# Kernel optimization log

Hardware: AMD Instinct MI355X
Metric: run time of the kernel (lower is better)

## Reference

```python
import jax, jax.numpy as jnp
import numpy as np

B, T, D, H, L = 64, 512, 1024, 1024, 2


def _make_params(key, in_size, hidden):
    # 4 input-to-hidden and 4 hidden-to-hidden matrices, gate order (i, f, n, o),
    # concatenated along the output axis -> one GEMM per source per step.
    k1, k2 = jax.random.split(key)
    sx = (6.0 / (in_size + hidden)) ** 0.5   # xavier_uniform bound
    sh = (6.0 / (hidden + hidden)) ** 0.5
    Wx = jax.random.uniform(k1, (in_size, 4 * hidden), minval=-sx, maxval=sx, dtype=jnp.float32)
    Wh = jax.random.uniform(k2, (hidden, 4 * hidden), minval=-sh, maxval=sh, dtype=jnp.float32)
    b = jnp.zeros((4 * hidden,), dtype=jnp.float32)
    return Wx, Wh, b


def setup_inputs() -> dict:
    key = jax.random.key(0)
    kx, k0, k1 = jax.random.split(key, 3)
    x = jax.random.normal(kx, (B, T, D), dtype=jnp.float32)
    h0 = jnp.zeros((L, B, H), dtype=jnp.float32)
    c0 = jnp.zeros((L, B, H), dtype=jnp.float32)
    Wx0, Wh0, b0 = _make_params(k0, D, H)
    Wx1, Wh1, b1 = _make_params(k1, H, H)
    return {"x": x, "h0": h0, "c0": c0,
            "Wx0": Wx0, "Wh0": Wh0, "b0": b0,
            "Wx1": Wx1, "Wh1": Wh1, "b1": b1}


def _run_layer(xseq, h, c, Wx, Wh, b):
    # xseq: [T, B, in], h/c: [B, H]
    def step(carry, xt):
        h, c = carry
        g = xt @ Wx + h @ Wh + b                       # [B, 4H]
        i_t, f_t, n_t, o_t = jnp.split(g, 4, axis=-1)
        i_t = jax.nn.sigmoid(i_t)
        f_t = jax.nn.sigmoid(f_t)
        n_t = jnp.tanh(n_t)
        o_t = jax.nn.sigmoid(o_t)
        c = f_t * c + i_t * n_t
        h = o_t * jnp.tanh(c)
        return (h, c), h
    (h, c), ys = jax.lax.scan(step, (h, c), xseq)
    return ys, h, c                                     # ys: [T, B, H]


def reference(x, h0, c0, Wx0, Wh0, b0, Wx1, Wh1, b1):
    xs = jnp.transpose(x, (1, 0, 2))                    # [T, B, D]
    params = [(Wx0, Wh0, b0), (Wx1, Wh1, b1)]
    hs, cs = [], []
    for layer in range(L):
        Wx, Wh, b = params[layer]
        xs, h, c = _run_layer(xs, h0[layer], c0[layer], Wx, Wh, b)
        hs.append(h)
        cs.append(c)
    outputs = jnp.transpose(xs, (1, 0, 2))              # [B, T, H]
    return outputs, (jnp.stack(hs, 0), jnp.stack(cs, 0))
```

## Files before the change

kernel.cpp:

```cpp
#include <hip/hip_runtime.h>


#define NBLK 256
#define TPB  512
#define T_   512
#define HS_OFF 33554432
#define CS_OFF 33685504

typedef float  f32x4  __attribute__((ext_vector_type(4)));
typedef short  bf16x8 __attribute__((ext_vector_type(8)));

#define WS_CTR  0u
#define WS_W    139264u
#define WS_BIAS 33693696u
#define WS_XB   33726464u
#define WS_H0   100835328u
#define WS_H1   101097472u
#define WS_MIN  101359616u

__device__ __forceinline__ unsigned short f2bf(float f) {
  union { float f; unsigned u; } v; v.f = f;
  return (unsigned short)((v.u + 0x7FFFu + ((v.u >> 16) & 1u)) >> 16);
}
__device__ __forceinline__ float fsig(float x) { return 1.0f / (1.0f + __expf(-x)); }
__device__ __forceinline__ float ftanh(float x) {
  x = fminf(15.0f, fmaxf(-15.0f, x));
  float e = __expf(2.0f * x);
  return (e - 1.0f) / (e + 1.0f);
}

__global__ void kw(const float* __restrict__ Wx0, const float* __restrict__ Wh0,
                   const float* __restrict__ Wx1, const float* __restrict__ Wh1,
                   unsigned short* __restrict__ wp) {
  __shared__ float tile[64][65];
  int tb = blockIdx.x;
  int m  = tb >> 10;
  int kt = (tb >> 6) & 15;
  int nt = tb & 63;
  const float* W = (m == 0) ? Wx0 : (m == 1) ? Wh0 : (m == 2) ? Wx1 : Wh1;
  unsigned short* O = wp + (size_t)m * 4194304u;
  int k0 = kt * 64, n0 = nt * 64;
  int tx = threadIdx.x & 63, tg = threadIdx.x >> 6;
  for (int r = tg; r < 64; r += 4)
    tile[r][tx] = W[(size_t)(k0 + r) * 4096 + n0 + tx];
  __syncthreads();
  for (int r = tg; r < 64; r += 4) {
    int n = n0 + r;
    int p = ((n & 1023) << 2) | (n >> 10);
    O[(size_t)p * 1024 + k0 + tx] = f2bf(tile[tx][r]);
  }
}

__global__ void kx(const float* __restrict__ x, unsigned short* __restrict__ xb) {
  int row = blockIdx.x;
  int t = row >> 6, b = row & 63;
  const float4* src = (const float4*)(x + ((size_t)b * 512 + t) * 1024);
  float4 f = src[threadIdx.x];
  ushort4 o; o.x = f2bf(f.x); o.y = f2bf(f.y); o.z = f2bf(f.z); o.w = f2bf(f.w);
  ((ushort4*)(xb + (size_t)row * 1024))[threadIdx.x] = o;
}

__global__ void kmisc(const float* __restrict__ b0, const float* __restrict__ b1,
                      const float* __restrict__ h0in,
                      float* __restrict__ biasP,
                      unsigned short* __restrict__ h0r, unsigned short* __restrict__ h1r) {
  int idx = blockIdx.x * 256 + threadIdx.x;
  if (idx < 8192) {
    int layer = idx >> 12, p = idx & 4095;
    int orig = (p & 3) * 1024 + (p >> 2);
    biasP[idx] = (layer ? b1 : b0)[orig];
  } else if (idx < 139264) {
    int e = idx - 8192;
    int layer = e >> 16, o = e & 65535;
    int row = o >> 10, col = o & 1023;
    unsigned short v = f2bf(h0in[layer * 65536 + o]);
    int dst = 65536 + (col >> 3) * 512 + row * 8 + (col & 7);
    if (layer) h1r[dst] = v; else h0r[dst] = v;
  }
}

__global__ void __launch_bounds__(TPB, 2)
klstm(const float* __restrict__ c0_in,
      const unsigned short* __restrict__ wp,
      const float* __restrict__ biasP,
      const unsigned short* __restrict__ xb,
      unsigned short* __restrict__ h0ring,
      unsigned short* __restrict__ h1ring,
      unsigned* __restrict__ ctrbase,
      float* __restrict__ out) {
  extern __shared__ char smem[];
  float* red  = (float*)(smem + 131072);
  float* lhb  = (float*)(smem + 139264);
  float* xred = (float*)(smem + 141312);
  unsigned* gctr  = ctrbase;
  unsigned* rctr  = ctrbase + 16384;
  unsigned* gflag = ctrbase + 17408;
  const int tid = threadIdx.x;
  const int w   = tid >> 6;
  const int l   = tid & 63;
  const int bid = blockIdx.x;
  const int n0  = bid * 16;
  const int layer = w >> 2;
  const int rbase = (w & 3) * 16;
  const int khalf = (w >> 2) * 512;
  const int grp   = bid >> 4;
  float* lh = lhb + w * 64;

  {
    const int msrc[4] = {0, 2, 1, 3};
    for (int s = 0; s < 4; ++s) {
      const char* src = (const char*)(wp + (size_t)msrc[s] * 4194304u + (size_t)n0 * 1024u);
      char* dst = smem + s * 32768;
      for (int i = tid; i < 2048; i += TPB) {
        int sb = i << 4;
        int c  = sb >> 11;
        int kb = sb & 2047;
        *(uint4*)(dst + (c << 11) + (kb ^ ((c & 7) << 4))) = *(const uint4*)(src + sb);
      }
    }
  }

  const int jg = bid * 4 + ((l & 15) >> 2);
  const float biasv = biasP[layer * 4096 + n0 + (l & 15)];
  const int qb = l & ~3;

  float cr[4];
  #pragma unroll
  for (int v = 0; v < 4; ++v)
    cr[v] = c0_in[layer * 65536 + (rbase + (l >> 4) * 4 + v) * 1024 + jg];

  const int ae0  = (rbase + (l & 15)) * 1024 + khalf + (l >> 4) * 8;
  const int hbase = ((khalf >> 3) + (l >> 4)) * 512 + (rbase + (l & 15)) * 8;
  const int lb0  = (l & 15) << 11;
  const int kb2  = khalf * 2 + (l >> 4) * 16;
  const int swz  = (l & 7) << 4;
  const int hsto = (bid >> 1) * 512 + 4 * (bid & 1);

  __syncthreads();

  f32x4 xacc = {0.f, 0.f, 0.f, 0.f};
  {
    #pragma unroll
    for (int kk = 0; kk < 16; ++kk) {
      bf16x8 ax = *(const bf16x8*)(xb + ae0 + kk * 32);
      bf16x8 b  = *(const bf16x8*)(smem + lb0 + ((kb2 + kk * 64) ^ swz));
      xacc = __builtin_amdgcn_mfma_f32_16x16x32_bf16(ax, b, xacc, 0, 0, 0);
    }
    if (w >= 4) {
      float* xr = xred + (size_t)(w & 3) * 256 + (size_t)l * 4;
      #pragma unroll
      for (int v = 0; v < 4; ++v) xr[v] = xacc[v];
    }
  }
  __syncthreads();

  for (int k = 0; k <= T_; ++k) {
    const unsigned short* h0p = h0ring + ((k + 1) & 1) * 65536;
    const unsigned short* h1p = h1ring + (k & 1) * 65536;

    bf16x8 hf0[16], hf1[16];
    #pragma unroll
    for (int kk = 0; kk < 16; ++kk) {
      const unsigned short* a0p = h0p + hbase + kk * 2048;
      const unsigned short* a1p = h1p + hbase + kk * 2048;
      asm volatile("global_load_dwordx4 %0, %1, off sc0 sc1"
                   : "=v"(hf0[kk]) : "v"(a0p));
      asm volatile("global_load_dwordx4 %0, %1, off sc0 sc1"
                   : "=v"(hf1[kk]) : "v"(a1p));
    }
    asm volatile("s_waitcnt vmcnt(0)" ::: "memory");
    __builtin_amdgcn_sched_barrier(0);

    f32x4 acc0  = {0.f, 0.f, 0.f, 0.f};
    f32x4 acc1a = {0.f, 0.f, 0.f, 0.f};
    f32x4 acc1b = {0.f, 0.f, 0.f, 0.f};
    #pragma unroll
    for (int kk = 0; kk < 16; ++kk) {
      const int bo = lb0 + ((kb2 + kk * 64) ^ swz);
      bf16x8 bh0 = *(const bf16x8*)(smem + 65536 + bo);
      bf16x8 bx1 = *(const bf16x8*)(smem + 32768 + bo);
      bf16x8 bh1 = *(const bf16x8*)(smem + 98304 + bo);
      acc0  = __builtin_amdgcn_mfma_f32_16x16x32_bf16(hf0[kk], bh0, acc0, 0, 0, 0);
      acc1a = __builtin_amdgcn_mfma_f32_16x16x32_bf16(hf0[kk], bx1, acc1a, 0, 0, 0);
      acc1b = __builtin_amdgcn_mfma_f32_16x16x32_bf16(hf1[kk], bh1, acc1b, 0, 0, 0);
    }

    {
      float* rb = red + (size_t)(w * 64 + l) * 4;
      f32x4 other = layer ? acc0 : (acc1a + acc1b);
      #pragma unroll
      for (int v = 0; v < 4; ++v) rb[v] = other[v];
    }
    __syncthreads();

    f32x4 g = layer ? (acc1a + acc1b) : acc0;
    {
      const int pw = layer ? (w - 4) : (w + 4);
      const float* rb = red + (size_t)(pw * 64 + l) * 4;
      #pragma unroll
      for (int v = 0; v < 4; ++v) g[v] += rb[v];
    }
    if (w < 4) {
      const float* xr = xred + (size_t)w * 256 + (size_t)l * 4;
      #pragma unroll
      for (int v = 0; v < 4; ++v) g[v] += xacc[v] + xr[v];
    }

    const bool active = layer ? (k >= 1) : (k < T_);
    f32x4 outv = {0.f, 0.f, 0.f, 0.f};
    if (active) {
      unsigned short* hw = layer ? (h1ring + ((k + 1) & 1) * 65536)
                                 : (h0ring + (k & 1) * 65536);
      #pragma unroll
      for (int v = 0; v < 4; ++v) {
        float gv = g[v] + biasv;
        float gi = __shfl(gv, qb);
        float gf = __shfl(gv, qb | 1);
        float gn = __shfl(gv, qb | 2);
        float go = __shfl(gv, qb | 3);
        float i_ = fsig(gi), f_ = fsig(gf), n_ = ftanh(gn), o_ = fsig(go);
        float c = f_ * cr[v] + i_ * n_;
        cr[v] = c;
        float h = o_ * ftanh(c);
        if ((l & 3) == 0)
          lh[((l >> 4) * 4 + v) * 4 + ((l & 15) >> 2)] = h;
      }
      if (l < 16) {
        f32x4 h4 = *(f32x4*)(lh + l * 4);
        outv = h4;
        ushort4 u4;
        u4.x = f2bf(h4[0]); u4.y = f2bf(h4[1]); u4.z = f2bf(h4[2]); u4.w = f2bf(h4[3]);
        union { ushort4 s; unsigned long long q; } pk; pk.s = u4;
        __hip_atomic_store((unsigned long long*)(hw + hsto + (rbase + l) * 8), pk.q,
                           __ATOMIC_RELAXED, __HIP_MEMORY_SCOPE_AGENT);
      }
    }

    if (k < T_) {
      __syncthreads();
      if (tid == 0) {
        unsigned old = __hip_atomic_fetch_add(&gctr[grp * 1024 + k], 1u,
                                              __ATOMIC_RELAXED, __HIP_MEMORY_SCOPE_AGENT);
        if (old == 15u) {
          unsigned oldr = __hip_atomic_fetch_add(&rctr[k], 1u,
                                                 __ATOMIC_RELAXED, __HIP_MEMORY_SCOPE_AGENT);
          if (oldr == 15u) {
            #pragma unroll
            for (int gg = 0; gg < 16; ++gg)
              __hip_atomic_store(&gflag[gg * 1024 + k], 1u,
                                 __ATOMIC_RELAXED, __HIP_MEMORY_SCOPE_AGENT);
          }
        }
      }
    }

    if (active && l < 16) {
      const int row = rbase + l;
      if (layer) {
        *(f32x4*)(out + (size_t)row * 524288u + (size_t)(k - 1) * 1024u + bid * 4) = outv;
        if (k == T_)
          *(f32x4*)(out + HS_OFF + 65536 + row * 1024 + bid * 4) = outv;
      } else if (k == T_ - 1) {
        *(f32x4*)(out + HS_OFF + row * 1024 + bid * 4) = outv;
      }
    }
    if (k + 1 < T_) {
      const unsigned short* xt = xb + (size_t)(k + 1) * 65536u;
      f32x4 xa = {0.f, 0.f, 0.f, 0.f};
      #pragma unroll
      for (int kk = 0; kk < 16; ++kk) {
        bf16x8 ax = *(const bf16x8*)(xt + ae0 + kk * 32);
        bf16x8 b  = *(const bf16x8*)(smem + lb0 + ((kb2 + kk * 64) ^ swz));
        xa = __builtin_amdgcn_mfma_f32_16x16x32_bf16(ax, b, xa, 0, 0, 0);
      }
      if (w >= 4) {
        float* xr = xred + (size_t)(w & 3) * 256 + (size_t)l * 4;
        #pragma unroll
        for (int v = 0; v < 4; ++v) xr[v] = xa[v];
      } else {
        xacc = xa;
      }
    }

    if (k < T_) {
      if (tid == 0) {
        unsigned spins = 0;
        while (__hip_atomic_load(&gflag[grp * 1024 + k], __ATOMIC_RELAXED, __HIP_MEMORY_SCOPE_AGENT) == 0u) {
          __builtin_amdgcn_s_sleep(1);
          if (++spins > 67108864u) break;
        }
      }
      __syncthreads();
    }
  }

  if ((l & 3) == 0) {
    #pragma unroll
    for (int v = 0; v < 4; ++v)
      out[CS_OFF + layer * 65536 + (rbase + (l >> 4) * 4 + v) * 1024 + jg] = cr[v];
  }
}

extern "C" void kernel_launch(void* const* d_in, const int* in_sizes, int n_in,
                              void* d_out, int out_size, void* d_ws, size_t ws_size,
                              hipStream_t stream) {
  const float* x   = (const float*)d_in[0];
  const float* h0  = (const float*)d_in[1];
  const float* c0  = (const float*)d_in[2];
  const float* Wx0 = (const float*)d_in[3];
  const float* Wh0 = (const float*)d_in[4];
  const float* b0  = (const float*)d_in[5];
  const float* Wx1 = (const float*)d_in[6];
  const float* Wh1 = (const float*)d_in[7];
  const float* b1  = (const float*)d_in[8];
  float* out = (float*)d_out;
  char* ws = (char*)d_ws;
  if (ws_size < (size_t)WS_MIN) return;

  unsigned* ctr       = (unsigned*)(ws + WS_CTR);
  unsigned short* wp  = (unsigned short*)(ws + WS_W);
  float* biasP        = (float*)(ws + WS_BIAS);
  unsigned short* xbp = (unsigned short*)(ws + WS_XB);
  unsigned short* h0r = (unsigned short*)(ws + WS_H0);
  unsigned short* h1r = (unsigned short*)(ws + WS_H1);

  (void)hipMemsetAsync(ctr, 0, 139264, stream);
  hipLaunchKernelGGL(kw,    dim3(4096),  dim3(256), 0, stream, Wx0, Wh0, Wx1, Wh1, wp);
  hipLaunchKernelGGL(kx,    dim3(32768), dim3(256), 0, stream, x, xbp);
  hipLaunchKernelGGL(kmisc, dim3(544),   dim3(256), 0, stream, b0, b1, h0, biasP, h0r, h1r);

  (void)hipFuncSetAttribute((const void*)klstm, hipFuncAttributeMaxDynamicSharedMemorySize, 145408);
  const float* c0a = c0; const unsigned short* wpa = wp; const float* bpa = biasP;
  const unsigned short* xba = xbp;
  unsigned short* h0a = h0r; unsigned short* h1a = h1r;
  unsigned* ca = ctr; float* oa = out;
  void* args[] = {&c0a, &wpa, &bpa, &xba, &h0a, &h1a, &ca, &oa};
  hipError_t e = hipLaunchCooperativeKernel((const void*)klstm, dim3(NBLK), dim3(TPB),
                                            args, 145408, stream);
  if (e != hipSuccess) {
    hipLaunchKernelGGL(klstm, dim3(NBLK), dim3(TPB), 145408, stream,
                       c0a, wpa, bpa, xba, h0a, h1a, ca, oa);
  }
}
```

Before: 4.792 ms.

## Halve persistent LSTM grid, give each block 32 gate columns, stream Wx from global

```diff
diff --git a/kernel.cpp b/kernel.cpp
--- a/kernel.cpp
+++ b/kernel.cpp
@@ -1,7 +1,7 @@
 #include <hip/hip_runtime.h>
 
 
-#define NBLK 256
+#define NBLK 128
 #define TPB  512
 #define T_   512
 #define HS_OFF 33554432
@@ -11,12 +11,13 @@
 typedef short  bf16x8 __attribute__((ext_vector_type(8)));
 
 #define WS_CTR  0u
-#define WS_W    139264u
-#define WS_BIAS 33693696u
-#define WS_XB   33726464u
-#define WS_H0   100835328u
-#define WS_H1   101097472u
-#define WS_MIN  101359616u
+#define WS_W    69632u
+#define WS_WXF  33624064u
+#define WS_BIAS 50401280u
+#define WS_XB   50434048u
+#define WS_H0   117542912u
+#define WS_H1   117805056u
+#define WS_MIN  118067200u
 
 __device__ __forceinline__ unsigned short f2bf(float f) {
   union { float f; unsigned u; } v; v.f = f;
@@ -51,6 +52,20 @@
   }
 }
 
+__global__ void kwf(const unsigned short* __restrict__ wp, unsigned short* __restrict__ wxf) {
+  int unit = blockIdx.x * 4 + (threadIdx.x >> 6);
+  int lane = threadIdx.x & 63;
+  int m  = unit >> 13;
+  int r  = unit & 8191;
+  int g  = r >> 5;
+  int kh = (r >> 4) & 1;
+  int kk = r & 15;
+  const char* src = (const char*)wp + (size_t)m * 16777216u
+                  + (size_t)(g * 16 + (lane & 15)) * 2048 + kh * 1024 + kk * 64 + (lane >> 4) * 16;
+  char* dst = (char*)wxf + (size_t)m * 8388608 + (size_t)((g * 2 + kh) * 16 + kk) * 1024 + lane * 16;
+  *(uint4*)dst = *(const uint4*)src;
+}
+
 __global__ void kx(const float* __restrict__ x, unsigned short* __restrict__ xb) {
   int row = blockIdx.x;
   int t = row >> 6, b = row & 63;
@@ -82,6 +97,7 @@
 __global__ void __launch_bounds__(TPB, 2)
 klstm(const float* __restrict__ c0_in,
       const unsigned short* __restrict__ wp,
+      const unsigned short* __restrict__ wxf,
       const float* __restrict__ biasP,
       const unsigned short* __restrict__ xb,
       unsigned short* __restrict__ h0ring,
@@ -89,67 +105,75 @@
       unsigned* __restrict__ ctrbase,
       float* __restrict__ out) {
   extern __shared__ char smem[];
-  float* red  = (float*)(smem + 131072);
-  float* lhb  = (float*)(smem + 139264);
-  float* xred = (float*)(smem + 141312);
+  float* redF  = (float*)(smem + 131072);
+  float* xredF = (float*)(smem + 147456);
+  float* lhF   = (float*)(smem + 155648);
   unsigned* gctr  = ctrbase;
-  unsigned* rctr  = ctrbase + 16384;
-  unsigned* gflag = ctrbase + 17408;
+  unsigned* rctr  = ctrbase + 8192;
+  unsigned* gflag = ctrbase + 9216;
   const int tid = threadIdx.x;
   const int w   = tid >> 6;
   const int l   = tid & 63;
-  const int bid = blockIdx.x;
-  const int n0  = bid * 16;
-  const int layer = w >> 2;
-  const int rbase = (w & 3) * 16;
-  const int khalf = (w >> 2) * 512;
-  const int grp   = bid >> 4;
-  float* lh = lhb + w * 64;
-
-  {
-    const int msrc[4] = {0, 2, 1, 3};
-    for (int s = 0; s < 4; ++s) {
-      const char* src = (const char*)(wp + (size_t)msrc[s] * 4194304u + (size_t)n0 * 1024u);
-      char* dst = smem + s * 32768;
-      for (int i = tid; i < 2048; i += TPB) {
-        int sb = i << 4;
-        int c  = sb >> 11;
-        int kb = sb & 2047;
-        *(uint4*)(dst + (c << 11) + (kb ^ ((c & 7) << 4))) = *(const uint4*)(src + sb);
-      }
-    }
-  }
-
-  const int jg = bid * 4 + ((l & 15) >> 2);
-  const float biasv = biasP[layer * 4096 + n0 + (l & 15)];
+  const int b   = blockIdx.x;
+  const int n0  = b * 32;
+  const int rt  = w & 3;
+  const int kh  = w >> 2;
+  const int rbase = rt * 16;
+  const int khalf = kh * 512;
+  const int grp   = b >> 4;
+
+  for (int s = 0; s < 2; ++s) {
+    const char* src = (const char*)wp + (size_t)(s ? 3u : 1u) * 8388608u + (size_t)n0 * 2048u;
+    char* dst = smem + s * 65536;
+    for (int i = tid; i < 4096; i += TPB) {
+      int sb = i << 4;
+      int c  = sb >> 11;
+      int kb = sb & 2047;
+      *(uint4*)(dst + (c << 11) + (kb ^ ((c & 7) << 4))) = *(const uint4*)(src + sb);
+    }
+  }
+
+  const float bias0 = biasP[kh * 4096 + n0 + (l & 15)];
+  const float bias1 = biasP[kh * 4096 + n0 + 16 + (l & 15)];
   const int qb = l & ~3;
-
-  float cr[4];
+  const int jg0 = b * 8 + ((l & 15) >> 2);
+  const int jg1 = jg0 + 4;
+
+  float cr0[4], cr1[4];
   #pragma unroll
-  for (int v = 0; v < 4; ++v)
-    cr[v] = c0_in[layer * 65536 + (rbase + (l >> 4) * 4 + v) * 1024 + jg];
-
-  const int ae0  = (rbase + (l & 15)) * 1024 + khalf + (l >> 4) * 8;
+  for (int v = 0; v < 4; ++v) {
+    int row = rbase + (l >> 4) * 4 + v;
+    cr0[v] = c0_in[kh * 65536 + row * 1024 + jg0];
+    cr1[v] = c0_in[kh * 65536 + row * 1024 + jg1];
+  }
+
+  const int ae0   = (rbase + (l & 15)) * 1024 + khalf + (l >> 4) * 8;
   const int hbase = ((khalf >> 3) + (l >> 4)) * 512 + (rbase + (l & 15)) * 8;
-  const int lb0  = (l & 15) << 11;
-  const int kb2  = khalf * 2 + (l >> 4) * 16;
-  const int swz  = (l & 7) << 4;
-  const int hsto = (bid >> 1) * 512 + 4 * (bid & 1);
+  const int kb2   = khalf * 2 + (l >> 4) * 16;
+  const int swz   = (l & 7) << 4;
+  const int cb0   = (l & 15) << 11;
+  const int cb1   = (16 + (l & 15)) << 11;
+  const char* wx1f0 = (const char*)wxf + 8388608 + (size_t)(b * 4 + kh) * 16384;
+  const char* wx1f1 = (const char*)wxf + 8388608 + (size_t)(b * 4 + 2 + kh) * 16384;
+  const char* wx0f0 = (const char*)wxf + (size_t)(b * 4 + kh) * 16384;
+  const char* wx0f1 = (const char*)wxf + (size_t)(b * 4 + 2 + kh) * 16384;
 
   __syncthreads();
 
-  f32x4 xacc = {0.f, 0.f, 0.f, 0.f};
+  f32x4 xacc0 = {0.f,0.f,0.f,0.f}, xacc1 = {0.f,0.f,0.f,0.f};
   {
     #pragma unroll
     for (int kk = 0; kk < 16; ++kk) {
       bf16x8 ax = *(const bf16x8*)(xb + ae0 + kk * 32);
-      bf16x8 b  = *(const bf16x8*)(smem + lb0 + ((kb2 + kk * 64) ^ swz));
-      xacc = __builtin_amdgcn_mfma_f32_16x16x32_bf16(ax, b, xacc, 0, 0, 0);
-    }
-    if (w >= 4) {
-      float* xr = xred + (size_t)(w & 3) * 256 + (size_t)l * 4;
+      bf16x8 b0 = *(const bf16x8*)(wx0f0 + kk * 1024 + l * 16);
+      bf16x8 b1 = *(const bf16x8*)(wx0f1 + kk * 1024 + l * 16);
+      xacc0 = __builtin_amdgcn_mfma_f32_16x16x32_bf16(ax, b0, xacc0, 0, 0, 0);
+      xacc1 = __builtin_amdgcn_mfma_f32_16x16x32_bf16(ax, b1, xacc1, 0, 0, 0);
+    }
+    if (kh) {
+      float* xr = xredF + (size_t)rt * 512 + (size_t)l * 8;
       #pragma unroll
-      for (int v = 0; v < 4; ++v) xr[v] = xacc[v];
+      for (int v = 0; v < 4; ++v) { xr[v] = xacc0[v]; xr[4 + v] = xacc1[v]; }
     }
   }
   __syncthreads();
@@ -163,76 +187,99 @@
     for (int kk = 0; kk < 16; ++kk) {
       const unsigned short* a0p = h0p + hbase + kk * 2048;
       const unsigned short* a1p = h1p + hbase + kk * 2048;
-      asm volatile("global_load_dwordx4 %0, %1, off sc0 sc1"
-                   : "=v"(hf0[kk]) : "v"(a0p));
-      asm volatile("global_load_dwordx4 %0, %1, off sc0 sc1"
-                   : "=v"(hf1[kk]) : "v"(a1p));
+      asm volatile("global_load_dwordx4 %0, %1, off sc0 sc1" : "=v"(hf0[kk]) : "v"(a0p));
+      asm volatile("global_load_dwordx4 %0, %1, off sc0 sc1" : "=v"(hf1[kk]) : "v"(a1p));
     }
     asm volatile("s_waitcnt vmcnt(0)" ::: "memory");
     __builtin_amdgcn_sched_barrier(0);
 
-    f32x4 acc0  = {0.f, 0.f, 0.f, 0.f};
-    f32x4 acc1a = {0.f, 0.f, 0.f, 0.f};
-    f32x4 acc1b = {0.f, 0.f, 0.f, 0.f};
+    f32x4 a00 = {0.f,0.f,0.f,0.f}, a01 = {0.f,0.f,0.f,0.f};
+    f32x4 ax0 = {0.f,0.f,0.f,0.f}, ax1 = {0.f,0.f,0.f,0.f};
+    f32x4 ah0 = {0.f,0.f,0.f,0.f}, ah1 = {0.f,0.f,0.f,0.f};
     #pragma unroll
     for (int kk = 0; kk < 16; ++kk) {
-      const int bo = lb0 + ((kb2 + kk * 64) ^ swz);
-      bf16x8 bh0 = *(const bf16x8*)(smem + 65536 + bo);
-      bf16x8 bx1 = *(const bf16x8*)(smem + 32768 + bo);
-      bf16x8 bh1 = *(const bf16x8*)(smem + 98304 + bo);
-      acc0  = __builtin_amdgcn_mfma_f32_16x16x32_bf16(hf0[kk], bh0, acc0, 0, 0, 0);
-      acc1a = __builtin_amdgcn_mfma_f32_16x16x32_bf16(hf0[kk], bx1, acc1a, 0, 0, 0);
-      acc1b = __builtin_amdgcn_mfma_f32_16x16x32_bf16(hf1[kk], bh1, acc1b, 0, 0, 0);
+      const int ko = (kb2 + kk * 64) ^ swz;
+      bf16x8 bh00 = *(const bf16x8*)(smem + cb0 + ko);
+      bf16x8 bh01 = *(const bf16x8*)(smem + cb1 + ko);
+      bf16x8 bh10 = *(const bf16x8*)(smem + 65536 + cb0 + ko);
+      bf16x8 bh11 = *(const bf16x8*)(smem + 65536 + cb1 + ko);
+      bf16x8 bx10 = *(const bf16x8*)(wx1f0 + kk * 1024 + l * 16);
+      bf16x8 bx11 = *(const bf16x8*)(wx1f1 + kk * 1024 + l * 16);
+      a00 = __builtin_amdgcn_mfma_f32_16x16x32_bf16(hf0[kk], bh00, a00, 0, 0, 0);
+      a01 = __builtin_amdgcn_mfma_f32_16x16x32_bf16(hf0[kk], bh01, a01, 0, 0, 0);
+      ax0 = __builtin_amdgcn_mfma_f32_16x16x32_bf16(hf0[kk], bx10, ax0, 0, 0, 0);
+      ax1 = __builtin_amdgcn_mfma_f32_16x16x32_bf16(hf0[kk], bx11, ax1, 0, 0, 0);
+      ah0 = __builtin_amdgcn_mfma_f32_16x16x32_bf16(hf1[kk], bh10, ah0, 0, 0, 0);
+      ah1 = __builtin_amdgcn_mfma_f32_16x16x32_bf16(hf1[kk], bh11, ah1, 0, 0, 0);
     }
 
     {
-      float* rb = red + (size_t)(w * 64 + l) * 4;
-      f32x4 other = layer ? acc0 : (acc1a + acc1b);
-      #pragma unroll
-      for (int v = 0; v < 4; ++v) rb[v] = other[v];
+      float* rb = redF + (size_t)w * 512 + (size_t)l * 8;
+      if (kh == 0) {
+        #pragma unroll
+        for (int v = 0; v < 4; ++v) { rb[v] = ax0[v] + ah0[v]; rb[4 + v] = ax1[v] + ah1[v]; }
+      } else {
+        #pragma unroll
+        for (int v = 0; v < 4; ++v) { rb[v] = a00[v]; rb[4 + v] = a01[v]; }
+      }
     }
     __syncthreads();
 
-    f32x4 g = layer ? (acc1a + acc1b) : acc0;
+    f32x4 g0, g1;
     {
-      const int pw = layer ? (w - 4) : (w + 4);
-      const float* rb = red + (size_t)(pw * 64 + l) * 4;
-      #pragma unroll
-      for (int v = 0; v < 4; ++v) g[v] += rb[v];
-    }
-    if (w < 4) {
-      const float* xr = xred + (size_t)w * 256 + (size_t)l * 4;
-      #pragma unroll
-      for (int v = 0; v < 4; ++v) g[v] += xacc[v] + xr[v];
-    }
-
-    const bool active = layer ? (k >= 1) : (k < T_);
-    f32x4 outv = {0.f, 0.f, 0.f, 0.f};
+      const float* rb = redF + (size_t)(w ^ 4) * 512 + (size_t)l * 8;
+      if (kh == 0) {
+        const float* xr = xredF + (size_t)rt * 512 + (size_t)l * 8;
+        #pragma unroll
+        for (int v = 0; v < 4; ++v) {
+          g0[v] = a00[v] + rb[v]     + xacc0[v] + xr[v];
+          g1[v] = a01[v] + rb[4 + v] + xacc1[v] + xr[4 + v];
+        }
+      } else {
+        #pragma unroll
+        for (int v = 0; v < 4; ++v) {
+          g0[v] = ax0[v] + ah0[v] + rb[v];
+          g1[v] = ax1[v] + ah1[v] + rb[4 + v];
+        }
+      }
+    }
+
+    const bool active = kh ? (k >= 1) : (k < T_);
+    f32x4 outA = {0.f,0.f,0.f,0.f}, outB = {0.f,0.f,0.f,0.f};
     if (active) {
-      unsigned short* hw = layer ? (h1ring + ((k + 1) & 1) * 65536)
-                                 : (h0ring + (k & 1) * 65536);
+      unsigned short* hw = kh ? (h1ring + ((k + 1) & 1) * 65536)
+                              : (h0ring + (k & 1) * 65536);
       #pragma unroll
       for (int v = 0; v < 4; ++v) {
-        float gv = g[v] + biasv;
-        float gi = __shfl(gv, qb);
-        float gf = __shfl(gv, qb | 1);
-        float gn = __shfl(gv, qb | 2);
-        float go = __shfl(gv, qb | 3);
-        float i_ = fsig(gi), f_ = fsig(gf), n_ = ftanh(gn), o_ = fsig(go);
-        float c = f_ * cr[v] + i_ * n_;
-        cr[v] = c;
-        float h = o_ * ftanh(c);
-        if ((l & 3) == 0)
-          lh[((l >> 4) * 4 + v) * 4 + ((l & 15) >> 2)] = h;
+        float gv0 = g0[v] + bias0;
+        float i0 = fsig(__shfl(gv0, qb)), f0 = fsig(__shfl(gv0, qb | 1));
+        float n0_ = ftanh(__shfl(gv0, qb | 2)), o0 = fsig(__shfl(gv0, qb | 3));
+        float c0v = f0 * cr0[v] + i0 * n0_;
+        cr0[v] = c0v;
+        float h0v = o0 * ftanh(c0v);
+        float gv1 = g1[v] + bias1;
+        float i1 = fsig(__shfl(gv1, qb)), f1 = fsig(__shfl(gv1, qb | 1));
+        float n1_ = ftanh(__shfl(gv1, qb | 2)), o1 = fsig(__shfl(gv1, qb | 3));
+        float c1v = f1 * cr1[v] + i1 * n1_;
+        cr1[v] = c1v;
+        float h1v = o1 * ftanh(c1v);
+        if ((l & 3) == 0) {
+          int row = (l >> 4) * 4 + v;
+          lhF[w * 128 + row * 8 + ((l & 15) >> 2)]     = h0v;
+          lhF[w * 128 + row * 8 + 4 + ((l & 15) >> 2)] = h1v;
+        }
       }
       if (l < 16) {
-        f32x4 h4 = *(f32x4*)(lh + l * 4);
-        outv = h4;
-        ushort4 u4;
-        u4.x = f2bf(h4[0]); u4.y = f2bf(h4[1]); u4.z = f2bf(h4[2]); u4.w = f2bf(h4[3]);
-        union { ushort4 s; unsigned long long q; } pk; pk.s = u4;
-        __hip_atomic_store((unsigned long long*)(hw + hsto + (rbase + l) * 8), pk.q,
-                           __ATOMIC_RELAXED, __HIP_MEMORY_SCOPE_AGENT);
+        f32x4 hA = *(f32x4*)(lhF + w * 128 + l * 8);
+        f32x4 hB = *(f32x4*)(lhF + w * 128 + l * 8 + 4);
+        outA = hA; outB = hB;
+        ushort4 uA, uB;
+        uA.x = f2bf(hA[0]); uA.y = f2bf(hA[1]); uA.z = f2bf(hA[2]); uA.w = f2bf(hA[3]);
+        uB.x = f2bf(hB[0]); uB.y = f2bf(hB[1]); uB.z = f2bf(hB[2]); uB.w = f2bf(hB[3]);
+        union { ushort4 s; unsigned long long q; } pA, pB; pA.s = uA; pB.s = uB;
+        unsigned long long* dst = (unsigned long long*)(hw + b * 512 + (rbase + l) * 8);
+        __hip_atomic_store(dst,     pA.q, __ATOMIC_RELAXED, __HIP_MEMORY_SCOPE_AGENT);
+        __hip_atomic_store(dst + 1, pB.q, __ATOMIC_RELAXED, __HIP_MEMORY_SCOPE_AGENT);
       }
     }
 
@@ -244,9 +291,9 @@
         if (old == 15u) {
           unsigned oldr = __hip_atomic_fetch_add(&rctr[k], 1u,
                                                  __ATOMIC_RELAXED, __HIP_MEMORY_SCOPE_AGENT);
-          if (oldr == 15u) {
+          if (oldr == 7u) {
             #pragma unroll
-            for (int gg = 0; gg < 16; ++gg)
+            for (int gg = 0; gg < 8; ++gg)
               __hip_atomic_store(&gflag[gg * 1024 + k], 1u,
                                  __ATOMIC_RELAXED, __HIP_MEMORY_SCOPE_AGENT);
           }
@@ -256,29 +303,35 @@
 
     if (active && l < 16) {
       const int row = rbase + l;
-      if (layer) {
-        *(f32x4*)(out + (size_t)row * 524288u + (size_t)(k - 1) * 1024u + bid * 4) = outv;
-        if (k == T_)
-          *(f32x4*)(out + HS_OFF + 65536 + row * 1024 + bid * 4) = outv;
+      if (kh) {
+        float* o = out + (size_t)row * 524288u + (size_t)(k - 1) * 1024u + b * 8;
+        *(f32x4*)o = outA; *(f32x4*)(o + 4) = outB;
+        if (k == T_) {
+          float* h = out + HS_OFF + 65536 + row * 1024 + b * 8;
+          *(f32x4*)h = outA; *(f32x4*)(h + 4) = outB;
+        }
       } else if (k == T_ - 1) {
-        *(f32x4*)(out + HS_OFF + row * 1024 + bid * 4) = outv;
+        float* h = out + HS_OFF + row * 1024 + b * 8;
+        *(f32x4*)h = outA; *(f32x4*)(h + 4) = outB;
       }
     }
     if (k + 1 < T_) {
       const unsigned short* xt = xb + (size_t)(k + 1) * 65536u;
-      f32x4 xa = {0.f, 0.f, 0.f, 0.f};
+      f32x4 xa0 = {0.f,0.f,0.f,0.f}, xa1 = {0.f,0.f,0.f,0.f};
       #pragma unroll
       for (int kk = 0; kk < 16; ++kk) {
         bf16x8 ax = *(const bf16x8*)(xt + ae0 + kk * 32);
-        bf16x8 b  = *(const bf16x8*)(smem + lb0 + ((kb2 + kk * 64) ^ swz));
-        xa = __builtin_amdgcn_mfma_f32_16x16x32_bf16(ax, b, xa, 0, 0, 0);
-      }
-      if (w >= 4) {
-        float* xr = xred + (size_t)(w & 3) * 256 + (size_t)l * 4;
+        bf16x8 b0 = *(const bf16x8*)(wx0f0 + kk * 1024 + l * 16);
+        bf16x8 b1 = *(const bf16x8*)(wx0f1 + kk * 1024 + l * 16);
+        xa0 = __builtin_amdgcn_mfma_f32_16x16x32_bf16(ax, b0, xa0, 0, 0, 0);
+        xa1 = __builtin_amdgcn_mfma_f32_16x16x32_bf16(ax, b1, xa1, 0, 0, 0);
+      }
+      if (kh) {
+        float* xr = xredF + (size_t)rt * 512 + (size_t)l * 8;
         #pragma unroll
-        for (int v = 0; v < 4; ++v) xr[v] = xa[v];
+        for (int v = 0; v < 4; ++v) { xr[v] = xa0[v]; xr[4 + v] = xa1[v]; }
       } else {
-        xacc = xa;
+        xacc0 = xa0; xacc1 = xa1;
       }
     }
 
@@ -296,8 +349,11 @@
 
   if ((l & 3) == 0) {
     #pragma unroll
-    for (int v = 0; v < 4; ++v)
-      out[CS_OFF + layer * 65536 + (rbase + (l >> 4) * 4 + v) * 1024 + jg] = cr[v];
+    for (int v = 0; v < 4; ++v) {
+      int row = rbase + (l >> 4) * 4 + v;
+      out[CS_OFF + kh * 65536 + row * 1024 + jg0] = cr0[v];
+      out[CS_OFF + kh * 65536 + row * 1024 + jg1] = cr1[v];
+    }
   }
 }
 
@@ -319,26 +375,28 @@
 
   unsigned* ctr       = (unsigned*)(ws + WS_CTR);
   unsigned short* wp  = (unsigned short*)(ws + WS_W);
+  unsigned short* wxf = (unsigned short*)(ws + WS_WXF);
   float* biasP        = (float*)(ws + WS_BIAS);
   unsigned short* xbp = (unsigned short*)(ws + WS_XB);
   unsigned short* h0r = (unsigned short*)(ws + WS_H0);
   unsigned short* h1r = (unsigned short*)(ws + WS_H1);
 
-  (void)hipMemsetAsync(ctr, 0, 139264, stream);
+  (void)hipMemsetAsync(ctr, 0, 69632, stream);
   hipLaunchKernelGGL(kw,    dim3(4096),  dim3(256), 0, stream, Wx0, Wh0, Wx1, Wh1, wp);
+  hipLaunchKernelGGL(kwf,   dim3(4096),  dim3(256), 0, stream, wp, wxf);
   hipLaunchKernelGGL(kx,    dim3(32768), dim3(256), 0, stream, x, xbp);
   hipLaunchKernelGGL(kmisc, dim3(544),   dim3(256), 0, stream, b0, b1, h0, biasP, h0r, h1r);
 
-  (void)hipFuncSetAttribute((const void*)klstm, hipFuncAttributeMaxDynamicSharedMemorySize, 145408);
-  const float* c0a = c0; const unsigned short* wpa = wp; const float* bpa = biasP;
-  const unsigned short* xba = xbp;
+  (void)hipFuncSetAttribute((const void*)klstm, hipFuncAttributeMaxDynamicSharedMemorySize, 159744);
+  const float* c0a = c0; const unsigned short* wpa = wp; const unsigned short* wxa = wxf;
+  const float* bpa = biasP; const unsigned short* xba = xbp;
   unsigned short* h0a = h0r; unsigned short* h1a = h1r;
   unsigned* ca = ctr; float* oa = out;
-  void* args[] = {&c0a, &wpa, &bpa, &xba, &h0a, &h1a, &ca, &oa};
+  void* args[] = {&c0a, &wpa, &wxa, &bpa, &xba, &h0a, &h1a, &ca, &oa};
   hipError_t e = hipLaunchCooperativeKernel((const void*)klstm, dim3(NBLK), dim3(TPB),
-                                            args, 145408, stream);
+                                            args, 159744, stream);
   if (e != hipSuccess) {
-    hipLaunchKernelGGL(klstm, dim3(NBLK), dim3(TPB), 145408, stream,
-                       c0a, wpa, bpa, xba, h0a, h1a, ca, oa);
-  }
-}
+    hipLaunchKernelGGL(klstm, dim3(NBLK), dim3(TPB), 159744, stream,
+                       c0a, wpa, wxa, bpa, xba, h0a, h1a, ca, oa);
+  }
+}
```

After: 12.37 ms. 158% more time.
